# Performance work log

Hardware: AMD Instinct MI355X
Metric: run time of the kernel (lower is better)

Reference implementation:

```python
import jax, jax.numpy as jnp
import numpy as np

B, J, DIMS, T = 1024, 22, 3, 100
C = J * DIMS            # 66 channels
H, HD = 8, 64           # heads, head_dim
E = H * HD              # 512
LOCAL_WINDOW = 5
EPS = 1e-5


def setup_inputs() -> dict:
    key = jax.random.key(0)
    ks = jax.random.split(key, 32)
    s = 0.02  # small init scale for learned params

    # kinematic-chain skeleton adjacency mask (buffer, symmetric 0/1)
    am = np.zeros((J, J), dtype=np.float32)
    for i in range(J - 1):
        am[i, i + 1] = 1.0
        am[i + 1, i] = 1.0
    adj_mask = jnp.asarray(am)

    # banded temporal mask: tril(+w) * triu(-w)
    tm = np.tril(np.ones((T, T), np.float32), LOCAL_WINDOW) * np.triu(np.ones((T, T), np.float32), -LOCAL_WINDOW)
    traj_mask = jnp.asarray(tm)

    def lin(k, din, dout):
        k1, k2 = jax.random.split(k)
        return (jax.random.normal(k1, (din, dout), jnp.float32) * s,
                jax.random.normal(k2, (dout,), jnp.float32) * s)

    # spatial->temporal attention: query_dim=C (66), key_dim=T (100)
    st_wq, st_bq = lin(ks[1], C, E)
    st_wk, st_bk = lin(ks[2], T, E)
    st_wv, st_bv = lin(ks[3], T, E)
    st_wo, st_bo = lin(ks[4], E, C)
    # temporal->spatial attention: query_dim=T (100), key_dim=C (66)
    ts_wq, ts_bq = lin(ks[5], T, E)
    ts_wk, ts_bk = lin(ks[6], C, E)
    ts_wv, ts_bv = lin(ks[7], C, E)
    ts_wo, ts_bo = lin(ks[8], E, T)

    return {
        "x": jax.random.normal(ks[0], (B, C, T), jnp.float32),
        "adj_mask": adj_mask,
        "s_adj": jnp.eye(J, dtype=jnp.float32),  # torch init: eye
        "traj_mask": traj_mask,
        # torch init is zeros; use small random so the temporal branch is non-degenerate
        "t_adj": jax.random.normal(ks[9], (T, T), jnp.float32) * s,
        "st_wq": st_wq, "st_bq": st_bq, "st_wk": st_wk, "st_bk": st_bk,
        "st_wv": st_wv, "st_bv": st_bv, "st_wo": st_wo, "st_bo": st_bo,
        "ts_wq": ts_wq, "ts_bq": ts_bq, "ts_wk": ts_wk, "ts_bk": ts_bk,
        "ts_wv": ts_wv, "ts_bv": ts_bv, "ts_wo": ts_wo, "ts_bo": ts_bo,
        "ln_alpha": jnp.ones((1, C, 1), jnp.float32),
        "ln_beta": jnp.zeros((1, C, 1), jnp.float32),
        "fc_w": jax.random.normal(ks[10], (T, T), jnp.float32) * s,  # torch Linear weight [out,in]
        "fc_b": jax.random.normal(ks[11], (T,), jnp.float32) * s,
    }


def _cross_attn(q, kv, wq, bq, wk, bk, wv, bv, wo, bo):
    # q: [B, Lq, qdim], kv: [B, Lk, kdim] -> [B, Lq, qdim]
    b = q.shape[0]
    Q = (q @ wq + bq).reshape(b, -1, H, HD)
    K = (kv @ wk + bk).reshape(b, -1, H, HD)
    V = (kv @ wv + bv).reshape(b, -1, H, HD)
    scores = jnp.einsum('bqhd,bkhd->bhqk', Q, K) / jnp.sqrt(jnp.float32(HD))
    attn = jax.nn.softmax(scores, axis=-1)
    out = jnp.einsum('bhqk,bkhd->bqhd', attn, V).reshape(b, -1, E)
    return out @ wo + bo


def reference(x, adj_mask, s_adj, traj_mask, t_adj,
              st_wq, st_bq, st_wk, st_bk, st_wv, st_bv, st_wo, st_bo,
              ts_wq, ts_bq, ts_wk, ts_bk, ts_wv, ts_bv, ts_wo, ts_bo,
              ln_alpha, ln_beta, fc_w, fc_b):
    b, c, t = x.shape
    j = c // DIMS

    # --- SpatialGC: symmetric degree-normalized masked adjacency conv ---
    deg = adj_mask.sum(axis=1)
    dis = jnp.where(deg > 0, deg ** -0.5, 0.0)
    A = s_adj * (adj_mask * dis[:, None] * dis[None, :])        # [J,J]
    spatial = jnp.einsum('vj,bjct->bvct', A, x.reshape(b, j, DIMS, t)).reshape(b, c, t)

    # --- TemporalGC: banded learned temporal adjacency ---
    temporal = jnp.einsum('ft,bnt->bnf', t_adj * traj_mask, x)   # [B,C,T]

    # --- CrossAttentiveGC ---
    sp_seq = spatial.transpose(0, 2, 1)                          # [B,T,C] spatial tokens
    tp_seq = temporal                                            # [B,C,T] temporal tokens
    enh_sp = _cross_attn(sp_seq, tp_seq, st_wq, st_bq, st_wk, st_bk, st_wv, st_bv, st_wo, st_bo)  # [B,T,C]
    enh_tp = _cross_attn(tp_seq, sp_seq, ts_wq, ts_bq, ts_wk, ts_bk, ts_wv, ts_bv, ts_wo, ts_bo)  # [B,C,T]
    combined = (enh_sp.reshape(b, t, j, DIMS).transpose(0, 2, 3, 1)
                + enh_tp.reshape(b, j, DIMS, t)).reshape(b, c, t)

    # --- LN over channel dim (dim=1) with biased variance ---
    mean = combined.mean(axis=1, keepdims=True)
    var = ((combined - mean) ** 2).mean(axis=1, keepdims=True)
    y = (combined - mean) / jnp.sqrt(var + EPS)
    y = y * ln_alpha + ln_beta

    # --- residual + Linear over the seq dim, tanh ---
    out = jnp.einsum('bct,ft->bcf', y + x, fc_w) + fc_b
    return jnp.tanh(out)
```

## Files before the change

### kernel.cpp

```cpp
#include <hip/hip_runtime.h>
#include <hip/hip_bf16.h>
#include <math.h>
#include <stdint.h>

typedef __hip_bfloat16 bf16;
typedef __attribute__((ext_vector_type(8))) short short8;
typedef __attribute__((ext_vector_type(4))) short short4v;
typedef __attribute__((ext_vector_type(4))) float f32x4;
typedef __attribute__((ext_vector_type(4))) unsigned int uint4v;
union PF { uint4v u; short8 s; };

#define CC 66
#define TT 100
#define JJ 22
#define HH 8
#define HD 64
#define EE 512
#define CPAD 101

#define SPT_R 112
#define SPT_S 96
#define TP_R 80
#define TP_S 128

#define W_STWK 0
#define W_STWQ 65536
#define W_TSWK 114688
#define W_TSWQ 163840
#define W_VST  229376
#define W_VTS  311296
#define W_TOTAL 397312

#define TOKSP 0
#define TOKTP 11648
#define G0Z1  22528
#define G0Z2  27648
#define G0Z3  34816
#define G1Z1  45056
#define G1Z2  52224
#define G1Z3  57344
#define SMEM_SH 71680

__device__ __forceinline__ bf16 f2b(float v){ return __float2bfloat16(v); }
__device__ __forceinline__ short sb(float v){ __hip_bfloat16 h = __float2bfloat16(v); return *(short*)&h; }
__device__ __forceinline__ unsigned int pk2(float a, float b){
  unsigned short ua = (unsigned short)sb(a), ub = (unsigned short)sb(b);
  return (unsigned int)ua | ((unsigned int)ub << 16);
}

__device__ __forceinline__ void tr_body(
    const float* __restrict__ src, bf16* __restrict__ dst,
    int Rsrc, int Csrc, int JP, int IP, int blk, int tid)
{
  int o = blk*256 + tid;
  if (o >= JP*IP) return;
  int j = o / IP, i = o - j*IP;
  float v = (j < Csrc && i < Rsrc) ? src[(long)i*Csrc + j] : 0.f;
  dst[o] = f2b(v);
}

__device__ __forceinline__ void wt_body(
    const float* __restrict__ wv, const float* __restrict__ wo,
    bf16* __restrict__ dst, int OUT, int KDIM, int OP, int KP, int blk, int tid)
{
  int idx = blk*256 + tid;
  if (idx >= 8*OP*KP) return;
  int o = idx % OP;
  int hk = idx / OP;
  int k = hk % KP, h = hk / KP;
  float acc = 0.f;
  if (o < OUT && k < KDIM) {
    const float* wvp = wv + (long)k*EE + h*64;
    const float* wop = wo + (long)(h*64)*OUT + o;
    #pragma unroll 8
    for (int d = 0; d < 64; ++d) acc += wvp[d] * wop[(long)d*OUT];
  }
  dst[(long)h*OP*KP + (long)o*KP + k] = f2b(acc);
}

__global__ __launch_bounds__(256) void k_wprep(
    const float* __restrict__ st_wk, const float* __restrict__ st_wq,
    const float* __restrict__ ts_wk, const float* __restrict__ ts_wq,
    const float* __restrict__ st_wv, const float* __restrict__ st_wo,
    const float* __restrict__ ts_wv, const float* __restrict__ ts_wo,
    const float* __restrict__ st_bo, const float* __restrict__ st_bv,
    const float* __restrict__ ts_bo, const float* __restrict__ ts_bv,
    bf16* __restrict__ wsec, float* __restrict__ bias2)
{
  const int blk = blockIdx.x, tid = threadIdx.x;
  if      (blk <  256) tr_body(st_wk, wsec + W_STWK, TT, EE, EE, 128, blk,      tid);
  else if (blk <  448) tr_body(st_wq, wsec + W_STWQ, CC, EE, EE,  96, blk-256,  tid);
  else if (blk <  640) tr_body(ts_wk, wsec + W_TSWK, CC, EE, EE,  96, blk-448,  tid);
  else if (blk <  896) tr_body(ts_wq, wsec + W_TSWQ, TT, EE, EE, 128, blk-640,  tid);
  else if (blk < 1216) wt_body(st_wv, st_wo, wsec + W_VST, CC, TT,  80, 128, blk-896,  tid);
  else if (blk < 1552) wt_body(ts_wv, ts_wo, wsec + W_VTS, TT, CC, 112,  96, blk-1216, tid);
  else {
    if (tid < 128) {
      int c = tid; float a = 0.f;
      if (c < CC) {
        a = st_bo[c];
        for (int e = 0; e < EE; ++e) a += st_bv[e] * st_wo[(long)e*CC + c];
      }
      bias2[tid] = a;
    } else {
      int t = tid - 128; float a = 0.f;
      if (t < TT) {
        a = ts_bo[t];
        for (int e = 0; e < EE; ++e) a += ts_bv[e] * ts_wo[(long)e*TT + t];
      }
      bias2[tid] = a;
    }
  }
}

__global__ __launch_bounds__(256) void k_prep(
    const float* __restrict__ x, const float* __restrict__ adj,
    const float* __restrict__ sadj, const float* __restrict__ tmask,
    const float* __restrict__ tadj,
    bf16* __restrict__ spT_all, bf16* __restrict__ tp_all)
{
  __shared__ float s_x[CC*TT];
  __shared__ float s_Mt[TT*TT];
  __shared__ float s_A[JJ*JJ];
  __shared__ float s_dis[JJ];
  const int b = blockIdx.x, tid = threadIdx.x;
  const long bb = (long)b * (CC*TT);

  if (tid < JJ) {
    float dsum = 0.f;
    for (int i = 0; i < JJ; ++i) dsum += adj[tid*JJ + i];
    s_dis[tid] = dsum > 0.f ? rsqrtf(dsum) : 0.f;
  }
  for (int o = tid; o < CC*TT; o += 256) s_x[o] = x[bb + o];
  for (int o = tid; o < TT*TT; o += 256) {
    int f = o / TT, t = o - f*TT;
    s_Mt[t*TT + f] = tadj[o] * tmask[o];
  }
  __syncthreads();
  for (int o = tid; o < JJ*JJ; o += 256) {
    int v = o / JJ, j = o - v*JJ;
    s_A[o] = sadj[o] * adj[o] * s_dis[v] * s_dis[j];
  }
  __syncthreads();

  bf16* spT = spT_all + (long)b * (SPT_R*SPT_S);
  bf16* tp  = tp_all  + (long)b * (TP_R*TP_S);

  for (int o = tid; o < 28*SPT_S; o += 256) {
    int t4 = o / SPT_S, c = o - t4*SPT_S;
    int t = t4*4;
    float ax=0.f, ay=0.f, az=0.f, aw=0.f;
    if (t < TT && c < CC) {
      int v = c/3, dd = c - v*3;
      for (int j = 0; j < JJ; ++j) {
        float av = s_A[v*JJ + j];
        float4 xv = *(const float4*)(s_x + (j*3+dd)*TT + t);
        ax += av*xv.x; ay += av*xv.y; az += av*xv.z; aw += av*xv.w;
      }
    }
    spT[(t  )*SPT_S + c] = f2b(ax);
    spT[(t+1)*SPT_S + c] = f2b(ay);
    spT[(t+2)*SPT_S + c] = f2b(az);
    spT[(t+3)*SPT_S + c] = f2b(aw);
  }
  for (int o = tid; o < TP_R*32; o += 256) {
    int n = o >> 5, f4 = o & 31;
    int f = f4*4;
    float ax=0.f, ay=0.f, az=0.f, aw=0.f;
    if (n < CC && f < TT) {
      for (int t = 0; t < TT; ++t) {
        float xv = s_x[n*TT + t];
        float4 w = *(const float4*)(s_Mt + t*TT + f);
        ax += xv*w.x; ay += xv*w.y; az += xv*w.z; aw += xv*w.w;
      }
    }
    short4v pk;
    pk.x = sb(ax); pk.y = sb(ay); pk.z = sb(az); pk.w = sb(aw);
    *(short4v*)(tp + n*TP_S + f) = pk;
  }
}

template<int Nt, int KCH, int SA, int SB>
__device__ __forceinline__ void build_kq(
    const short* __restrict__ W, const short* __restrict__ Tok,
    short* __restrict__ Z, const float* __restrict__ rowbias,
    int gw, int ln, int qd)
{
  const int mi = gw & 3;
  const int d0 = mi*16 + qd*4;
  const short* ap = W + (long)(mi*16 + ln)*SA;
  short8 af[KCH];
  #pragma unroll
  for (int kc = 0; kc < KCH; ++kc) af[kc] = *(const short8*)(ap + qd*8 + kc*32);
  float rb0=0.f, rb1=0.f, rb2=0.f, rb3=0.f;
  if (rowbias) { rb0=rowbias[d0]; rb1=rowbias[d0+1]; rb2=rowbias[d0+2]; rb3=rowbias[d0+3]; }
  constexpr int NU = (Nt + 1) / 2;
  #pragma unroll
  for (int u = 0; u < NU; ++u) {
    const int ni = (gw >> 2) + 2*u;
    if (ni < Nt) {
      const int row = ni*16 + ln;
      const short* bp = Tok + (long)row*SB;
      f32x4 acc = {0.f,0.f,0.f,0.f};
      #pragma unroll
      for (int kc = 0; kc < KCH; ++kc)
        acc = __builtin_amdgcn_mfma_f32_16x16x32_bf16(
            af[kc], *(const short8*)(bp + qd*8 + kc*32), acc, 0,0,0);
      short4v pk;
      pk.x = sb(acc[0]+rb0); pk.y = sb(acc[1]+rb1);
      pk.z = sb(acc[2]+rb2); pk.w = sb(acc[3]+rb3);
      *(short4v*)(Z + row*64 + (d0 ^ ((ln & 7) << 3))) = pk;
    }
  }
}

template<int Mt, int Nt, int KCH, int SA, int SB, int SZ>
__device__ __forceinline__ void build_vt(
    const short* __restrict__ Tok, const short* __restrict__ Wv,
    short* __restrict__ Z, int gw, int ln, int qd)
{
  if (gw >= Mt) return;
  const int mi = gw;
  const int k0 = mi*16 + qd*4;
  const short* ap = Tok + (long)(mi*16 + ln)*SA;
  short8 af[KCH];
  #pragma unroll
  for (int kc = 0; kc < KCH; ++kc) af[kc] = *(const short8*)(ap + qd*8 + kc*32);
  #pragma unroll
  for (int ni = 0; ni < Nt; ++ni) {
    const int row = ni*16 + ln;
    const short* bp = Wv + (long)row*SB;
    f32x4 acc = {0.f,0.f,0.f,0.f};
    #pragma unroll
    for (int kc = 0; kc < KCH; ++kc)
      acc = __builtin_amdgcn_mfma_f32_16x16x32_bf16(
          af[kc], *(const short8*)(bp + qd*8 + kc*32), acc, 0,0,0);
    short4v pk;
    pk.x = sb(acc[0]); pk.y = sb(acc[1]); pk.z = sb(acc[2]); pk.w = sb(acc[3]);
    *(short4v*)(Z + row*SZ + (k0 ^ ((ln & 7) << 3))) = pk;
  }
}

template<int A>
__device__ __forceinline__ void build_head(
    short* __restrict__ SMEM, const short* __restrict__ wsec,
    const float* __restrict__ bq, int h, int gw, int ln, int qd)
{
  constexpr int MQ  = A ? 5 : 7;
  constexpr int MKV = A ? 7 : 5;
  constexpr int MO  = A ? 7 : 5;
  constexpr int QCH = A ? 4 : 3;
  constexpr int KCH = A ? 3 : 4;
  constexpr int SWQ = A ? 128 : 96;
  constexpr int SWK = A ? 96 : 128;
  constexpr int SWV = A ? 96 : 128;
  constexpr int STQ = A ? 136 : 104;
  constexpr int STK = A ? 104 : 136;
  const short* tokq = SMEM + (A ? TOKTP : TOKSP);
  const short* tokk = SMEM + (A ? TOKSP : TOKTP);
  short* Z1 = SMEM + (A ? G1Z1 : G0Z1);
  short* Z2 = SMEM + (A ? G1Z2 : G0Z2);
  short* Z3 = SMEM + (A ? G1Z3 : G0Z3);
  const short* wkT = wsec + (A ? W_TSWK : W_STWK);
  const short* wqT = wsec + (A ? W_TSWQ : W_STWQ);
  const short* wvt = wsec + (A ? W_VTS  : W_VST);
  const int base = h * HD;
  build_kq<MKV, KCH, SWK, STK>(wkT + (long)base*SWK, tokk, Z1, nullptr, gw, ln, qd);
  build_kq<MQ,  QCH, SWQ, STQ>(wqT + (long)base*SWQ, tokq, Z2, bq + base, gw, ln, qd);
  build_vt<MKV, MO, KCH, STK, SWV, 128>(tokk, wvt + (long)h*(MO*16*SWV), Z3, gw, ln, qd);
}

template<int A>
__device__ __forceinline__ void chain_head(
    const short* __restrict__ SMEM, f32x4* __restrict__ accO,
    int gw, int ln, int qd)
{
  constexpr int KVR = A ? 100 : 66;
  constexpr int MQ  = A ? 5 : 7;
  constexpr int MKV = A ? 7 : 5;
  constexpr int MO  = A ? 7 : 5;
  constexpr int PCH = A ? 4 : 3;
  if (gw >= MQ) return;
  const short* Z1 = SMEM + (A ? G1Z1 : G0Z1);
  const short* Z2 = SMEM + (A ? G1Z2 : G0Z2);
  const short* Z3 = SMEM + (A ? G1Z3 : G0Z3);
  const int msk = (ln & 7) << 3;

  const short* bqp = Z2 + (gw*16 + ln)*64;
  const short8 qf0 = *(const short8*)(bqp + ((qd*8     ) ^ msk));
  const short8 qf1 = *(const short8*)(bqp + ((qd*8 + 32) ^ msk));
  f32x4 s[MKV];
  #pragma unroll
  for (int ni = 0; ni < MKV; ++ni) {
    const short* ap = Z1 + (ni*16 + ln)*64;
    f32x4 acc = {0.f,0.f,0.f,0.f};
    acc = __builtin_amdgcn_mfma_f32_16x16x32_bf16(
        *(const short8*)(ap + ((qd*8     ) ^ msk)), qf0, acc, 0,0,0);
    acc = __builtin_amdgcn_mfma_f32_16x16x32_bf16(
        *(const short8*)(ap + ((qd*8 + 32) ^ msk)), qf1, acc, 0,0,0);
    s[ni] = acc;
  }
  #pragma unroll
  for (int ni = 0; ni < MKV; ++ni) {
    #pragma unroll
    for (int r = 0; r < 4; ++r) {
      const int kv = ni*16 + qd*4 + r;
      s[ni][r] = (kv < KVR) ? s[ni][r]*0.125f : -1e30f;
    }
  }
  float mx = -1e30f;
  #pragma unroll
  for (int ni = 0; ni < MKV; ++ni)
    #pragma unroll
    for (int r = 0; r < 4; ++r) mx = fmaxf(mx, s[ni][r]);
  mx = fmaxf(mx, __shfl_xor(mx, 16));
  mx = fmaxf(mx, __shfl_xor(mx, 32));
  float l = 0.f;
  #pragma unroll
  for (int ni = 0; ni < MKV; ++ni)
    #pragma unroll
    for (int r = 0; r < 4; ++r) {
      float p = __expf(s[ni][r] - mx);
      s[ni][r] = p; l += p;
    }
  l += __shfl_xor(l, 16);
  l += __shfl_xor(l, 32);
  const float rs = 1.f / l;
  unsigned int plo[2*PCH], phi[2*PCH];
  #pragma unroll
  for (int ni = 0; ni < 2*PCH; ++ni) {
    if (ni < MKV) {
      plo[ni] = pk2(s[ni][0]*rs, s[ni][1]*rs);
      phi[ni] = pk2(s[ni][2]*rs, s[ni][3]*rs);
    } else { plo[ni] = 0u; phi[ni] = 0u; }
  }
  PF pf[PCH];
  #pragma unroll
  for (int kc = 0; kc < PCH; ++kc) {
    #pragma unroll
    for (int w = 0; w < 4; ++w) {
      const int srcLane = ln + 16*((qd & 1)*2 + (w >> 1));
      int va, vb;
      if (w & 1) {
        va = __shfl((int)phi[2*kc  ], srcLane, 64);
        vb = __shfl((int)phi[2*kc+1], srcLane, 64);
      } else {
        va = __shfl((int)plo[2*kc  ], srcLane, 64);
        vb = __shfl((int)plo[2*kc+1], srcLane, 64);
      }
      pf[kc].u[w] = (qd < 2) ? (unsigned int)va : (unsigned int)vb;
    }
  }
  #pragma unroll
  for (int oi = 0; oi < MO; ++oi) {
    const short* ap = Z3 + (oi*16 + ln)*128;
    f32x4 acc = accO[oi];
    #pragma unroll
    for (int kc = 0; kc < PCH; ++kc) {
      short8 af = *(const short8*)(ap + ((qd*8 + kc*32) ^ msk));
      acc = __builtin_amdgcn_mfma_f32_16x16x32_bf16(af, pf[kc].s, acc, 0,0,0);
    }
    accO[oi] = acc;
  }
}

__global__ __launch_bounds__(1024) void k_attn2(
    const bf16* __restrict__ spT_all, const bf16* __restrict__ tp_all,
    const bf16* __restrict__ wsec_,
    const float* __restrict__ st_bq, const float* __restrict__ ts_bq,
    const float* __restrict__ bias2, const float* __restrict__ x,
    const float* __restrict__ alpha, const float* __restrict__ beta,
    const float* __restrict__ fcw, const float* __restrict__ fcb,
    float* __restrict__ out)
{
  __shared__ __align__(16) short SMEM[SMEM_SH];
  const int b = blockIdx.x, tid = threadIdx.x;
  const long bb = (long)b * (CC*TT);
  const int wave = tid >> 6, lane = tid & 63, ln = lane & 15, qd = lane >> 4;
  const int g = wave >> 3, gw = wave & 7;
  const short* wsec = (const short*)wsec_;

  {
    const short* gsp = (const short*)(spT_all + (long)b*SPT_R*SPT_S);
    const short* gtp = (const short*)(tp_all  + (long)b*TP_R*TP_S);
    for (int o = tid; o < 112*12; o += 1024) {
      int r = o / 12, c8 = o - r*12;
      *(short8*)(SMEM + TOKSP + r*104 + c8*8) = *(const short8*)(gsp + r*SPT_S + c8*8);
    }
    for (int o = tid; o < 80*16; o += 1024) {
      int r = o >> 4, c8 = o & 15;
      *(short8*)(SMEM + TOKTP + r*136 + c8*8) = *(const short8*)(gtp + r*TP_S + c8*8);
    }
  }
  for (int o = tid; o < 80*16; o += 1024) {
    int r = o >> 4, kv = 80 + (o & 15);
    SMEM[G0Z3 + r*128 + (kv ^ ((r & 7) << 3))] = 0;
  }
  for (int o = tid; o < 112*16; o += 1024) {
    int r = o >> 4, kv = 112 + (o & 15);
    SMEM[G1Z3 + r*128 + (kv ^ ((r & 7) << 3))] = 0;
  }

  f32x4 accO[7];
  { f32x4 z = {0.f,0.f,0.f,0.f};
    #pragma unroll
    for (int i = 0; i < 7; ++i) accO[i] = z; }

  for (int h = 0; h < HH; ++h) {
    __syncthreads();
    if (g == 0) build_head<0>(SMEM, wsec, st_bq, h, gw, ln, qd);
    else        build_head<1>(SMEM, wsec, ts_bq, h, gw, ln, qd);
    __syncthreads();
    if (g == 0) chain_head<0>(SMEM, accO, gw, ln, qd);
    else        chain_head<1>(SMEM, accO, gw, ln, qd);
  }

  float* comb = (float*)(SMEM + G0Z1);
  float* s_w  = comb + 6668;
  __syncthreads();
  if (g == 0) {
    if (gw < 7) {
      const int t = gw*16 + ln;
      if (t < TT) {
        #pragma unroll
        for (int oi = 0; oi < 5; ++oi)
          #pragma unroll
          for (int r = 0; r < 4; ++r) {
            const int c = oi*16 + qd*4 + r;
            if (c < CC) comb[c*CPAD + t] = accO[oi][r];
          }
      }
    }
  } else {
    for (int o = tid - 512; o < TT*TT; o += 512) {
      int f = o / TT, t = o - f*TT;
      s_w[t*TT + f] = fcw[o];
    }
  }
  __syncthreads();
  if (g == 1 && gw < 5) {
    const int c = gw*16 + ln;
    if (c < CC) {
      #pragma unroll
      for (int oi = 0; oi < 7; ++oi)
        #pragma unroll
        for (int r = 0; r < 4; ++r) {
          const int t = oi*16 + qd*4 + r;
          if (t < TT) comb[c*CPAD + t] += accO[oi][r];
        }
    }
  }
  __syncthreads();
  for (int o = tid; o < CC*TT; o += 1024) {
    int c = o / TT, t = o - c*TT;
    comb[c*CPAD + t] += bias2[c] + bias2[128 + t];
  }
  __syncthreads();
  if (tid < 2*TT) {
    const int t = tid >> 1, hf = tid & 1;
    float part = 0.f;
    for (int c = hf; c < CC; c += 2) part += comb[c*CPAD + t];
    float mean = (part + __shfl_xor(part, 1)) * (1.f/CC);
    float vp = 0.f;
    for (int c = hf; c < CC; c += 2) { float dv = comb[c*CPAD + t] - mean; vp += dv*dv; }
    float var = (vp + __shfl_xor(vp, 1)) * (1.f/CC);
    float rstd = 1.f / sqrtf(var + 1e-5f);
    for (int c = hf; c < CC; c += 2) {
      float y = (comb[c*CPAD + t] - mean) * rstd * alpha[c] + beta[c];
      comb[c*CPAD + t] = y + x[bb + c*TT + t];
    }
  }
  __syncthreads();
  for (int o = tid; o < CC*25; o += 1024) {
    int c = o / 25, f4 = o - c*25;
    int f = f4*4;
    const float* cr = comb + c*CPAD;
    float ax=0.f, ay=0.f, az=0.f, aw=0.f;
    for (int t = 0; t < TT; ++t) {
      float xv = cr[t];
      float4 w = *(const float4*)(s_w + t*TT + f);
      ax += xv*w.x; ay += xv*w.y; az += xv*w.z; aw += xv*w.w;
    }
    float4 r4;
    r4.x = tanhf(ax + fcb[f  ]); r4.y = tanhf(ay + fcb[f+1]);
    r4.z = tanhf(az + fcb[f+2]); r4.w = tanhf(aw + fcb[f+3]);
    *(float4*)(out + bb + c*TT + f) = r4;
  }
}

__global__ __launch_bounds__(128) void k_fused(
    const float* __restrict__ x, const float* __restrict__ adj,
    const float* __restrict__ sadj, const float* __restrict__ tmask,
    const float* __restrict__ tadj,
    const float* __restrict__ st_wq, const float* __restrict__ st_bq,
    const float* __restrict__ st_wk, const float* __restrict__ st_bk,
    const float* __restrict__ st_wv, const float* __restrict__ st_bv,
    const float* __restrict__ st_wo, const float* __restrict__ st_bo,
    const float* __restrict__ ts_wq, const float* __restrict__ ts_bq,
    const float* __restrict__ ts_wk, const float* __restrict__ ts_bk,
    const float* __restrict__ ts_wv, const float* __restrict__ ts_bv,
    const float* __restrict__ ts_wo, const float* __restrict__ ts_bo,
    const float* __restrict__ alpha, const float* __restrict__ beta,
    const float* __restrict__ fcw, const float* __restrict__ fcb,
    float* __restrict__ out)
{
  __shared__ float s_sp[CC*TT];
  __shared__ float s_tp[CC*TT];
  __shared__ __align__(16) float s_kv[2*TT*HD];
  __shared__ float s_comb[CC*CPAD];
  __shared__ float s_A[JJ*JJ];
  __shared__ float s_dis[JJ];

  const int b = blockIdx.x, tid = threadIdx.x;
  const long bb = (long)b * (CC*TT);
  float* s_xs = s_comb;
  float* s_Mt = s_kv;

  if (tid < JJ) {
    float dsum = 0.f;
    for (int i = 0; i < JJ; ++i) dsum += adj[tid*JJ + i];
    s_dis[tid] = dsum > 0.f ? rsqrtf(dsum) : 0.f;
  }
  for (int o = tid; o < CC*TT; o += 128) s_xs[o] = x[bb + o];
  for (int o = tid; o < TT*TT; o += 128) {
    int f = o / TT, t = o - f*TT;
    s_Mt[t*TT + f] = tadj[o] * tmask[o];
  }
  __syncthreads();
  for (int o = tid; o < JJ*JJ; o += 128) {
    int v = o / JJ, j = o - v*JJ;
    s_A[o] = sadj[o] * adj[o] * s_dis[v] * s_dis[j];
  }
  __syncthreads();

  for (int o = tid; o < CC*TT; o += 128) {
    int c = o / TT, t = o - c*TT, v = c / 3, dd = c - v*3;
    float acc = 0.f;
    for (int j = 0; j < JJ; ++j) acc += s_A[v*JJ + j] * s_xs[(j*3 + dd)*TT + t];
    s_sp[o] = acc;
  }
  for (int o = tid; o < CC*TT; o += 128) {
    int n = o / TT, f = o - n*TT;
    float a0 = 0.f, a1 = 0.f;
    for (int t = 0; t < TT; t += 2) {
      a0 += s_xs[n*TT + t    ] * s_Mt[(t    )*TT + f];
      a1 += s_xs[n*TT + t + 1] * s_Mt[(t + 1)*TT + f];
    }
    s_tp[o] = a0 + a1;
  }
  __syncthreads();

  for (int o = tid; o < CC*TT; o += 128) {
    int c = o / TT, t = o - c*TT;
    s_comb[c*CPAD + t] = st_bo[c] + ts_bo[t];
  }

  {
    float* s_k = s_kv;
    float* s_v = s_kv + TT*HD;
    for (int h = 0; h < HH; ++h) {
      const int base = h*HD;
      __syncthreads();
      {
        const int d = tid & 63, krow = tid >> 6;
        for (int kk = 0; kk < CC/2; ++kk) {
          int k = kk*2 + krow;
          float aK = st_bk[base + d], aV = st_bv[base + d];
          const float* tr = s_tp + k*TT;
          for (int t = 0; t < TT; ++t) {
            float a = tr[t];
            aK += a * st_wk[(long)t*EE + base + d];
            aV += a * st_wv[(long)t*EE + base + d];
          }
          s_k[k*HD + d] = aK;
          s_v[k*HD + d] = aV;
        }
      }
      __syncthreads();
      if (tid < TT) {
        const int q = tid;
        float qv[HD];
        #pragma unroll
        for (int d = 0; d < HD; ++d) qv[d] = st_bq[base + d];
        for (int c = 0; c < CC; ++c) {
          float a = s_sp[c*TT + q];
          const float* wr = st_wq + (long)c*EE + base;
          #pragma unroll
          for (int d = 0; d < HD; ++d) qv[d] += a * wr[d];
        }
        float m = -INFINITY, l = 0.f, ov[HD];
        #pragma unroll
        for (int d = 0; d < HD; ++d) ov[d] = 0.f;
        for (int k = 0; k < CC; ++k) {
          const float4* kr4 = (const float4*)(s_k + k*HD);
          float s0=0.f,s1=0.f,s2=0.f,s3=0.f;
          #pragma unroll
          for (int i = 0; i < 16; ++i) {
            float4 kk4 = kr4[i];
            s0 += qv[4*i  ]*kk4.x; s1 += qv[4*i+1]*kk4.y;
            s2 += qv[4*i+2]*kk4.z; s3 += qv[4*i+3]*kk4.w;
          }
          float s  = (s0+s1+s2+s3) * 0.125f;
          float mn = fmaxf(m, s);
          float corr = __expf(m - mn);
          float p    = __expf(s - mn);
          l = l*corr + p;
          const float4* vr4 = (const float4*)(s_v + k*HD);
          #pragma unroll
          for (int i = 0; i < 16; ++i) {
            float4 vv4 = vr4[i];
            ov[4*i  ] = ov[4*i  ]*corr + p*vv4.x;
            ov[4*i+1] = ov[4*i+1]*corr + p*vv4.y;
            ov[4*i+2] = ov[4*i+2]*corr + p*vv4.z;
            ov[4*i+3] = ov[4*i+3]*corr + p*vv4.w;
          }
          m = mn;
        }
        float rl = 1.f/l;
        #pragma unroll
        for (int d = 0; d < HD; ++d) ov[d] *= rl;
        for (int c = 0; c < CC; ++c) {
          const float* wr = st_wo + (long)base*CC + c;
          float a0=0.f,a1=0.f,a2=0.f,a3=0.f;
          #pragma unroll
          for (int d = 0; d < HD; d += 4) {
            a0 += ov[d  ]*wr[(long)(d  )*CC]; a1 += ov[d+1]*wr[(long)(d+1)*CC];
            a2 += ov[d+2]*wr[(long)(d+2)*CC]; a3 += ov[d+3]*wr[(long)(d+3)*CC];
          }
          s_comb[c*CPAD + q] += a0+a1+a2+a3;
        }
      }
    }
  }

  {
    float* s_k = s_kv;
    float* s_v = s_kv + TT*HD;
    for (int h = 0; h < HH; ++h) {
      const int base = h*HD;
      __syncthreads();
      {
        const int d = tid & 63, krow = tid >> 6;
        for (int kk = 0; kk < TT/2; ++kk) {
          int k = kk*2 + krow;
          float aK = ts_bk[base + d], aV = ts_bv[base + d];
          for (int c = 0; c < CC; ++c) {
            float a = s_sp[c*TT + k];
            aK += a * ts_wk[(long)c*EE + base + d];
            aV += a * ts_wv[(long)c*EE + base + d];
          }
          s_k[k*HD + d] = aK;
          s_v[k*HD + d] = aV;
        }
      }
      __syncthreads();
      if (tid < CC) {
        const int q = tid;
        float qv[HD];
        #pragma unroll
        for (int d = 0; d < HD; ++d) qv[d] = ts_bq[base + d];
        const float* tr = s_tp + q*TT;
        for (int t = 0; t < TT; ++t) {
          float a = tr[t];
          const float* wr = ts_wq + (long)t*EE + base;
          #pragma unroll
          for (int d = 0; d < HD; ++d) qv[d] += a * wr[d];
        }
        float m = -INFINITY, l = 0.f, ov[HD];
        #pragma unroll
        for (int d = 0; d < HD; ++d) ov[d] = 0.f;
        for (int k = 0; k < TT; ++k) {
          const float4* kr4 = (const float4*)(s_k + k*HD);
          float s0=0.f,s1=0.f,s2=0.f,s3=0.f;
          #pragma unroll
          for (int i = 0; i < 16; ++i) {
            float4 kk4 = kr4[i];
            s0 += qv[4*i  ]*kk4.x; s1 += qv[4*i+1]*kk4.y;
            s2 += qv[4*i+2]*kk4.z; s3 += qv[4*i+3]*kk4.w;
          }
          float s  = (s0+s1+s2+s3) * 0.125f;
          float mn = fmaxf(m, s);
          float corr = __expf(m - mn);
          float p    = __expf(s - mn);
          l = l*corr + p;
          const float4* vr4 = (const float4*)(s_v + k*HD);
          #pragma unroll
          for (int i = 0; i < 16; ++i) {
            float4 vv4 = vr4[i];
            ov[4*i  ] = ov[4*i  ]*corr + p*vv4.x;
            ov[4*i+1] = ov[4*i+1]*corr + p*vv4.y;
            ov[4*i+2] = ov[4*i+2]*corr + p*vv4.z;
            ov[4*i+3] = ov[4*i+3]*corr + p*vv4.w;
          }
          m = mn;
        }
        float rl = 1.f/l;
        #pragma unroll
        for (int d = 0; d < HD; ++d) ov[d] *= rl;
        for (int t = 0; t < TT; ++t) {
          const float* wr = ts_wo + (long)base*TT + t;
          float a0=0.f,a1=0.f,a2=0.f,a3=0.f;
          #pragma unroll
          for (int d = 0; d < HD; d += 4) {
            a0 += ov[d  ]*wr[(long)(d  )*TT]; a1 += ov[d+1]*wr[(long)(d+1)*TT];
            a2 += ov[d+2]*wr[(long)(d+2)*TT]; a3 += ov[d+3]*wr[(long)(d+3)*TT];
          }
          s_comb[q*CPAD + t] += a0+a1+a2+a3;
        }
      }
    }
  }
  __syncthreads();

  if (tid < TT) {
    const int t = tid;
    float mean = 0.f;
    for (int c = 0; c < CC; ++c) mean += s_comb[c*CPAD + t];
    mean *= (1.f/CC);
    float var = 0.f;
    for (int c = 0; c < CC; ++c) { float dv = s_comb[c*CPAD + t] - mean; var += dv*dv; }
    var *= (1.f/CC);
    float rstd = 1.f / sqrtf(var + 1e-5f);
    for (int c = 0; c < CC; ++c) {
      float y = (s_comb[c*CPAD + t] - mean) * rstd * alpha[c] + beta[c];
      s_comb[c*CPAD + t] = y + x[bb + c*TT + t];
    }
  }
  __syncthreads();

  float* s_w = s_kv;
  for (int o = tid; o < TT*TT; o += 128) {
    int f = o / TT, t = o - f*TT;
    s_w[t*TT + f] = fcw[o];
  }
  __syncthreads();

  for (int o = tid; o < CC*TT; o += 128) {
    int c = o / TT, f = o - c*TT;
    const float* cr = s_comb + c*CPAD;
    float a0 = 0.f, a1 = 0.f;
    for (int t = 0; t < TT; t += 2) {
      a0 += cr[t    ] * s_w[(t    )*TT + f];
      a1 += cr[t + 1] * s_w[(t + 1)*TT + f];
    }
    out[bb + o] = tanhf(a0 + a1 + fcb[f]);
  }
}

extern "C" void kernel_launch(void* const* d_in, const int* in_sizes, int n_in,
                              void* d_out, int out_size, void* d_ws, size_t ws_size,
                              hipStream_t stream) {
  const float* x     = (const float*)d_in[0];
  const float* adj   = (const float*)d_in[1];
  const float* sadj  = (const float*)d_in[2];
  const float* tmask = (const float*)d_in[3];
  const float* tadj  = (const float*)d_in[4];
  const float* st_wq = (const float*)d_in[5];  const float* st_bq = (const float*)d_in[6];
  const float* st_wk = (const float*)d_in[7];  const float* st_bk = (const float*)d_in[8];
  const float* st_wv = (const float*)d_in[9];  const float* st_bv = (const float*)d_in[10];
  const float* st_wo = (const float*)d_in[11]; const float* st_bo = (const float*)d_in[12];
  const float* ts_wq = (const float*)d_in[13]; const float* ts_bq = (const float*)d_in[14];
  const float* ts_wk = (const float*)d_in[15]; const float* ts_bk = (const float*)d_in[16];
  const float* ts_wv = (const float*)d_in[17]; const float* ts_bv = (const float*)d_in[18];
  const float* ts_wo = (const float*)d_in[19]; const float* ts_bo = (const float*)d_in[20];
  const float* alpha = (const float*)d_in[21]; const float* beta  = (const float*)d_in[22];
  const float* fcw   = (const float*)d_in[23]; const float* fcb   = (const float*)d_in[24];
  float* out = (float*)d_out;

  const int B = in_sizes[0] / (CC*TT);
  const size_t w_bytes   = (size_t)W_TOTAL * 2 + 1024;
  const size_t spt_bytes = (size_t)B * SPT_R * SPT_S * 2;
  const size_t tp_bytes  = (size_t)B * TP_R * TP_S * 2;
  const size_t need = w_bytes + spt_bytes + tp_bytes;

  if (ws_size >= need) {
    bf16*  wsec    = (bf16*)d_ws;
    float* bias2   = (float*)((char*)d_ws + (size_t)W_TOTAL*2);
    bf16*  spT_all = (bf16*)((char*)d_ws + w_bytes);
    bf16*  tp_all  = spT_all + (size_t)B * SPT_R * SPT_S;

    k_wprep<<<1553, 256, 0, stream>>>(st_wk, st_wq, ts_wk, ts_wq,
                                      st_wv, st_wo, ts_wv, ts_wo,
                                      st_bo, st_bv, ts_bo, ts_bv,
                                      wsec, bias2);
    k_prep<<<B, 256, 0, stream>>>(x, adj, sadj, tmask, tadj, spT_all, tp_all);
    k_attn2<<<B, 1024, 0, stream>>>(spT_all, tp_all, wsec, st_bq, ts_bq,
                                    bias2, x, alpha, beta, fcw, fcb, out);
  } else {
    k_fused<<<B, 128, 0, stream>>>(x, adj, sadj, tmask, tadj,
                                   st_wq, st_bq, st_wk, st_bk, st_wv, st_bv, st_wo, st_bo,
                                   ts_wq, ts_bq, ts_wk, ts_bk, ts_wv, ts_bv, ts_wo, ts_bo,
                                   alpha, beta, fcw, fcb, out);
  }
}
```

Before: 675.2 us.

## Accumulate attention outputs into shared memory with atomics and swizzle LDS layouts

The per-head output projection no longer keeps 7 f32x4 accumulators in registers. It atomically adds each head's contribution straight into a shared-memory combined buffer, which removes the two-phase write/add epilogue and its extra barriers. The shared layouts also change: token and V buffers get XOR swizzles and tighter strides (128 and 96 instead of 136), aimed at fewer bank conflicts and less LDS use. The cost is 8 heads of LDS float atomics per element and a larger total LDS footprint from the new comb region.

```diff
diff --git a/kernel.cpp b/kernel.cpp
--- a/kernel.cpp
+++ b/kernel.cpp
@@ -17,6 +17,7 @@
 #define HD 64
 #define EE 512
 #define CPAD 101
+#define CPD 100
 
 #define SPT_R 112
 #define SPT_S 96
@@ -31,15 +32,16 @@
 #define W_VTS  311296
 #define W_TOTAL 397312
 
-#define TOKSP 0
-#define TOKTP 11648
-#define G0Z1  22528
-#define G0Z2  27648
-#define G0Z3  34816
-#define G1Z1  45056
-#define G1Z2  52224
-#define G1Z3  57344
-#define SMEM_SH 71680
+#define TSPo 0
+#define TTPo 11648
+#define K0Z  21888
+#define Q0Z  27008
+#define V0Z  34176
+#define K1Z  41856
+#define Q1Z  49024
+#define V1Z  54144
+#define CMB  68480
+#define SMEM2 81680
 
 __device__ __forceinline__ bf16 f2b(float v){ return __float2bfloat16(v); }
 __device__ __forceinline__ short sb(float v){ __hip_bfloat16 h = __float2bfloat16(v); return *(short*)&h; }
@@ -180,8 +182,8 @@
   }
 }
 
-template<int Nt, int KCH, int SA, int SB>
-__device__ __forceinline__ void build_kq(
+template<int Nt, int KCH, int SA, int SB, int SWBM>
+__device__ __forceinline__ void b_kq(
     const short* __restrict__ W, const short* __restrict__ Tok,
     short* __restrict__ Z, const float* __restrict__ rowbias,
     int gw, int ln, int qd)
@@ -194,6 +196,7 @@
   for (int kc = 0; kc < KCH; ++kc) af[kc] = *(const short8*)(ap + qd*8 + kc*32);
   float rb0=0.f, rb1=0.f, rb2=0.f, rb3=0.f;
   if (rowbias) { rb0=rowbias[d0]; rb1=rowbias[d0+1]; rb2=rowbias[d0+2]; rb3=rowbias[d0+3]; }
+  const int bsw = (ln & SWBM) << 3;
   constexpr int NU = (Nt + 1) / 2;
   #pragma unroll
   for (int u = 0; u < NU; ++u) {
@@ -205,7 +208,7 @@
       #pragma unroll
       for (int kc = 0; kc < KCH; ++kc)
         acc = __builtin_amdgcn_mfma_f32_16x16x32_bf16(
-            af[kc], *(const short8*)(bp + qd*8 + kc*32), acc, 0,0,0);
+            af[kc], *(const short8*)(bp + ((qd*8 + kc*32) ^ bsw)), acc, 0,0,0);
       short4v pk;
       pk.x = sb(acc[0]+rb0); pk.y = sb(acc[1]+rb1);
       pk.z = sb(acc[2]+rb2); pk.w = sb(acc[3]+rb3);
@@ -214,18 +217,20 @@
   }
 }
 
-template<int Mt, int Nt, int KCH, int SA, int SB, int SZ>
-__device__ __forceinline__ void build_vt(
+template<int Mt, int Nt, int KCH, int SA, int SWAM, int SB, int SZ, int SWZM>
+__device__ __forceinline__ void b_vt(
     const short* __restrict__ Tok, const short* __restrict__ Wv,
     short* __restrict__ Z, int gw, int ln, int qd)
 {
   if (gw >= Mt) return;
   const int mi = gw;
   const int k0 = mi*16 + qd*4;
+  const int asw = (ln & SWAM) << 3;
   const short* ap = Tok + (long)(mi*16 + ln)*SA;
   short8 af[KCH];
   #pragma unroll
-  for (int kc = 0; kc < KCH; ++kc) af[kc] = *(const short8*)(ap + qd*8 + kc*32);
+  for (int kc = 0; kc < KCH; ++kc)
+    af[kc] = *(const short8*)(ap + ((qd*8 + kc*32) ^ asw));
   #pragma unroll
   for (int ni = 0; ni < Nt; ++ni) {
     const int row = ni*16 + ln;
@@ -237,7 +242,7 @@
           af[kc], *(const short8*)(bp + qd*8 + kc*32), acc, 0,0,0);
     short4v pk;
     pk.x = sb(acc[0]); pk.y = sb(acc[1]); pk.z = sb(acc[2]); pk.w = sb(acc[3]);
-    *(short4v*)(Z + row*SZ + (k0 ^ ((ln & 7) << 3))) = pk;
+    *(short4v*)(Z + row*SZ + (k0 ^ ((ln & SWZM) << 3))) = pk;
   }
 }
 
@@ -254,37 +259,46 @@
   constexpr int SWQ = A ? 128 : 96;
   constexpr int SWK = A ? 96 : 128;
   constexpr int SWV = A ? 96 : 128;
-  constexpr int STQ = A ? 136 : 104;
-  constexpr int STK = A ? 104 : 136;
-  const short* tokq = SMEM + (A ? TOKTP : TOKSP);
-  const short* tokk = SMEM + (A ? TOKSP : TOKTP);
-  short* Z1 = SMEM + (A ? G1Z1 : G0Z1);
-  short* Z2 = SMEM + (A ? G1Z2 : G0Z2);
-  short* Z3 = SMEM + (A ? G1Z3 : G0Z3);
+  constexpr int STQ = A ? 128 : 104;
+  constexpr int SWQM= A ? 7 : 0;
+  constexpr int STK = A ? 104 : 128;
+  constexpr int SWKM= A ? 0 : 7;
+  constexpr int VS  = A ? 128 : 96;
+  constexpr int VWM = A ? 7 : 3;
+  const short* tokq = SMEM + (A ? TTPo : TSPo);
+  const short* tokk = SMEM + (A ? TSPo : TTPo);
+  short* Z1 = SMEM + (A ? K1Z : K0Z);
+  short* Z2 = SMEM + (A ? Q1Z : Q0Z);
+  short* Z3 = SMEM + (A ? V1Z : V0Z);
   const short* wkT = wsec + (A ? W_TSWK : W_STWK);
   const short* wqT = wsec + (A ? W_TSWQ : W_STWQ);
   const short* wvt = wsec + (A ? W_VTS  : W_VST);
   const int base = h * HD;
-  build_kq<MKV, KCH, SWK, STK>(wkT + (long)base*SWK, tokk, Z1, nullptr, gw, ln, qd);
-  build_kq<MQ,  QCH, SWQ, STQ>(wqT + (long)base*SWQ, tokq, Z2, bq + base, gw, ln, qd);
-  build_vt<MKV, MO, KCH, STK, SWV, 128>(tokk, wvt + (long)h*(MO*16*SWV), Z3, gw, ln, qd);
+  b_kq<MKV, KCH, SWK, STK, SWKM>(wkT + (long)base*SWK, tokk, Z1, nullptr, gw, ln, qd);
+  b_kq<MQ,  QCH, SWQ, STQ, SWQM>(wqT + (long)base*SWQ, tokq, Z2, bq + base, gw, ln, qd);
+  b_vt<MKV, MO, KCH, STK, SWKM, SWV, VS, VWM>(tokk, wvt + (long)h*(MO*16*SWV), Z3, gw, ln, qd);
 }
 
 template<int A>
 __device__ __forceinline__ void chain_head(
-    const short* __restrict__ SMEM, f32x4* __restrict__ accO,
-    int gw, int ln, int qd)
+    short* __restrict__ SMEM, int gw, int ln, int qd)
 {
   constexpr int KVR = A ? 100 : 66;
+  constexpr int QROWS = A ? 66 : 100;
+  constexpr int OUTD  = A ? 100 : 66;
   constexpr int MQ  = A ? 5 : 7;
   constexpr int MKV = A ? 7 : 5;
   constexpr int MO  = A ? 7 : 5;
   constexpr int PCH = A ? 4 : 3;
+  constexpr int VS  = A ? 128 : 96;
+  constexpr int VWM = A ? 7 : 3;
   if (gw >= MQ) return;
-  const short* Z1 = SMEM + (A ? G1Z1 : G0Z1);
-  const short* Z2 = SMEM + (A ? G1Z2 : G0Z2);
-  const short* Z3 = SMEM + (A ? G1Z3 : G0Z3);
+  const short* Z1 = SMEM + (A ? K1Z : K0Z);
+  const short* Z2 = SMEM + (A ? Q1Z : Q0Z);
+  const short* Z3 = SMEM + (A ? V1Z : V0Z);
+  float* comb = (float*)(SMEM + CMB);
   const int msk = (ln & 7) << 3;
+  const int vmsk = (ln & VWM) << 3;
 
   const short* bqp = Z2 + (gw*16 + ln)*64;
   const short8 qf0 = *(const short8*)(bqp + ((qd*8     ) ^ msk));
@@ -351,16 +365,25 @@
       pf[kc].u[w] = (qd < 2) ? (unsigned int)va : (unsigned int)vb;
     }
   }
+  const int q = gw*16 + ln;
   #pragma unroll
   for (int oi = 0; oi < MO; ++oi) {
-    const short* ap = Z3 + (oi*16 + ln)*128;
-    f32x4 acc = accO[oi];
+    const short* ap = Z3 + (oi*16 + ln)*VS;
+    f32x4 acc = {0.f,0.f,0.f,0.f};
     #pragma unroll
-    for (int kc = 0; kc < PCH; ++kc) {
-      short8 af = *(const short8*)(ap + ((qd*8 + kc*32) ^ msk));
-      acc = __builtin_amdgcn_mfma_f32_16x16x32_bf16(af, pf[kc].s, acc, 0,0,0);
-    }
-    accO[oi] = acc;
+    for (int kc = 0; kc < PCH; ++kc)
+      acc = __builtin_amdgcn_mfma_f32_16x16x32_bf16(
+          *(const short8*)(ap + ((qd*8 + kc*32) ^ vmsk)), pf[kc].s, acc, 0,0,0);
+    if (q < QROWS) {
+      #pragma unroll
+      for (int r = 0; r < 4; ++r) {
+        const int outc = oi*16 + qd*4 + r;
+        if (outc < OUTD) {
+          const int idx = A ? (q*CPD + outc) : (outc*CPD + q);
+          atomicAdd(&comb[idx], acc[r]);
+        }
+      }
+    }
   }
 }
 
@@ -373,113 +396,81 @@
     const float* __restrict__ fcw, const float* __restrict__ fcb,
     float* __restrict__ out)
 {
-  __shared__ __align__(16) short SMEM[SMEM_SH];
+  __shared__ __align__(16) short SMEM[SMEM2];
   const int b = blockIdx.x, tid = threadIdx.x;
   const long bb = (long)b * (CC*TT);
   const int wave = tid >> 6, lane = tid & 63, ln = lane & 15, qd = lane >> 4;
   const int g = wave >> 3, gw = wave & 7;
   const short* wsec = (const short*)wsec_;
+  float* comb = (float*)(SMEM + CMB);
 
   {
     const short* gsp = (const short*)(spT_all + (long)b*SPT_R*SPT_S);
     const short* gtp = (const short*)(tp_all  + (long)b*TP_R*TP_S);
     for (int o = tid; o < 112*12; o += 1024) {
       int r = o / 12, c8 = o - r*12;
-      *(short8*)(SMEM + TOKSP + r*104 + c8*8) = *(const short8*)(gsp + r*SPT_S + c8*8);
+      *(short8*)(SMEM + TSPo + r*104 + c8*8) = *(const short8*)(gsp + r*SPT_S + c8*8);
     }
     for (int o = tid; o < 80*16; o += 1024) {
       int r = o >> 4, c8 = o & 15;
-      *(short8*)(SMEM + TOKTP + r*136 + c8*8) = *(const short8*)(gtp + r*TP_S + c8*8);
-    }
+      *(short8*)(SMEM + TTPo + r*128 + ((c8*8) ^ ((r & 7) << 3))) =
+          *(const short8*)(gtp + r*TP_S + c8*8);
+    }
+    for (int o = tid; o < CC*CPD; o += 1024) comb[o] = 0.f;
   }
   for (int o = tid; o < 80*16; o += 1024) {
     int r = o >> 4, kv = 80 + (o & 15);
-    SMEM[G0Z3 + r*128 + (kv ^ ((r & 7) << 3))] = 0;
+    SMEM[V0Z + r*96 + (kv ^ ((r & 3) << 3))] = 0;
   }
   for (int o = tid; o < 112*16; o += 1024) {
     int r = o >> 4, kv = 112 + (o & 15);
-    SMEM[G1Z3 + r*128 + (kv ^ ((r & 7) << 3))] = 0;
-  }
-
-  f32x4 accO[7];
-  { f32x4 z = {0.f,0.f,0.f,0.f};
-    #pragma unroll
-    for (int i = 0; i < 7; ++i) accO[i] = z; }
+    SMEM[V1Z + r*128 + (kv ^ ((r & 7) << 3))] = 0;
+  }
 
   for (int h = 0; h < HH; ++h) {
     __syncthreads();
     if (g == 0) build_head<0>(SMEM, wsec, st_bq, h, gw, ln, qd);
     else        build_head<1>(SMEM, wsec, ts_bq, h, gw, ln, qd);
     __syncthreads();
-    if (g == 0) chain_head<0>(SMEM, accO, gw, ln, qd);
-    else        chain_head<1>(SMEM, accO, gw, ln, qd);
-  }
-
-  float* comb = (float*)(SMEM + G0Z1);
-  float* s_w  = comb + 6668;
-  __syncthreads();
-  if (g == 0) {
-    if (gw < 7) {
-      const int t = gw*16 + ln;
-      if (t < TT) {
-        #pragma unroll
-        for (int oi = 0; oi < 5; ++oi)
-          #pragma unroll
-          for (int r = 0; r < 4; ++r) {
-            const int c = oi*16 + qd*4 + r;
-            if (c < CC) comb[c*CPAD + t] = accO[oi][r];
-          }
-      }
-    }
-  } else {
-    for (int o = tid - 512; o < TT*TT; o += 512) {
-      int f = o / TT, t = o - f*TT;
-      s_w[t*TT + f] = fcw[o];
-    }
-  }
-  __syncthreads();
-  if (g == 1 && gw < 5) {
-    const int c = gw*16 + ln;
-    if (c < CC) {
-      #pragma unroll
-      for (int oi = 0; oi < 7; ++oi)
-        #pragma unroll
-        for (int r = 0; r < 4; ++r) {
-          const int t = oi*16 + qd*4 + r;
-          if (t < TT) comb[c*CPAD + t] += accO[oi][r];
-        }
-    }
-  }
-  __syncthreads();
+    if (g == 0) chain_head<0>(SMEM, gw, ln, qd);
+    else        chain_head<1>(SMEM, gw, ln, qd);
+  }
+
+  float* s_w = (float*)(SMEM + K0Z);
+  __syncthreads();
+  for (int o = tid; o < TT*TT; o += 1024) {
+    int f = o / TT, t = o - f*TT;
+    s_w[t*TT + f] = fcw[o];
+  }
   for (int o = tid; o < CC*TT; o += 1024) {
     int c = o / TT, t = o - c*TT;
-    comb[c*CPAD + t] += bias2[c] + bias2[128 + t];
+    comb[c*CPD + t] += bias2[c] + bias2[128 + t];
   }
   __syncthreads();
   if (tid < 2*TT) {
     const int t = tid >> 1, hf = tid & 1;
     float part = 0.f;
-    for (int c = hf; c < CC; c += 2) part += comb[c*CPAD + t];
+    for (int c = hf; c < CC; c += 2) part += comb[c*CPD + t];
     float mean = (part + __shfl_xor(part, 1)) * (1.f/CC);
     float vp = 0.f;
-    for (int c = hf; c < CC; c += 2) { float dv = comb[c*CPAD + t] - mean; vp += dv*dv; }
+    for (int c = hf; c < CC; c += 2) { float dv = comb[c*CPD + t] - mean; vp += dv*dv; }
     float var = (vp + __shfl_xor(vp, 1)) * (1.f/CC);
     float rstd = 1.f / sqrtf(var + 1e-5f);
     for (int c = hf; c < CC; c += 2) {
-      float y = (comb[c*CPAD + t] - mean) * rstd * alpha[c] + beta[c];
-      comb[c*CPAD + t] = y + x[bb + c*TT + t];
+      float y = (comb[c*CPD + t] - mean) * rstd * alpha[c] + beta[c];
+      comb[c*CPD + t] = y + x[bb + c*TT + t];
     }
   }
   __syncthreads();
   for (int o = tid; o < CC*25; o += 1024) {
     int c = o / 25, f4 = o - c*25;
     int f = f4*4;
-    const float* cr = comb + c*CPAD;
+    const float* cr = comb + c*CPD;
     float ax=0.f, ay=0.f, az=0.f, aw=0.f;
     for (int t = 0; t < TT; ++t) {
       float xv = cr[t];
-      float4 w = *(const float4*)(s_w + t*TT + f);
-      ax += xv*w.x; ay += xv*w.y; az += xv*w.z; aw += xv*w.w;
+      float4 wv = *(const float4*)(s_w + t*TT + f);
+      ax += xv*wv.x; ay += xv*wv.y; az += xv*wv.z; aw += xv*wv.w;
     }
     float4 r4;
     r4.x = tanhf(ax + fcb[f  ]); r4.y = tanhf(ay + fcb[f+1]);
```

Result: slower. 1.184 ms (+75.4%).
